# Kernel tuning notes

Hardware: AMD Instinct MI355X
Metric: run time of the kernel (lower is better)

Reference implementation:

```python
import jax, jax.numpy as jnp
import numpy as np
from jax import lax

B, N, NUM_Q, H = 16, 64, 256, 64


def setup_inputs() -> dict:
    key = jax.random.key(0)
    ks = jax.random.split(key, 12)
    s = 0.05
    return {
        "q": jax.random.randint(ks[0], (B, N), 0, NUM_Q),
        "r": jax.random.randint(ks[1], (B, N), 0, 2),
        "x_emb": jax.random.normal(ks[2], (2 * NUM_Q, H), jnp.float32) * s,
        "q_emb": jax.random.normal(ks[3], (NUM_Q, H), jnp.float32) * s,
        "init_h": jax.random.normal(ks[4], (NUM_Q, H), jnp.float32) * s,
        "w1": jax.random.normal(ks[5], (2 * H, H), jnp.float32) * s,
        "b1": jnp.zeros((H,), jnp.float32),
        "w2": jax.random.normal(ks[6], (H, H), jnp.float32) * s,
        "b2": jnp.zeros((H,), jnp.float32),
        "w_ih": jax.random.normal(ks[7], (3 * H, 2 * H), jnp.float32) * s,
        "w_hh": jax.random.normal(ks[8], (3 * H, H), jnp.float32) * s,
        "b_ih": jnp.zeros((3 * H,), jnp.float32),
        "b_hh": jnp.zeros((3 * H,), jnp.float32),
        "bias": jnp.zeros((1, NUM_Q, 1), jnp.float32),
        "out_w": jax.random.normal(ks[9], (H,), jnp.float32) * s,
        "theta": jnp.asarray(0.0, jnp.float32),
    }


def reference(q, r, x_emb, q_emb, init_h, w1, b1, w2, b2, w_ih, w_hh, b_ih, b_hh, bias, out_w, theta):
    xe = x_emb[q + NUM_Q * r]                          # [B,N,H]
    mask = jax.nn.one_hot(q, NUM_Q, dtype=xe.dtype)    # [B,N,Q] one-hot of answered KC
    ht0 = jnp.broadcast_to(init_h, (B, NUM_Q, H))

    def gru_seq(x):
        # torch nn.GRU(batch_first=True) scanned over the num_q axis, h0 = 0.
        # x: [B,Q,2H] -> [B,Q,H]; gate order (r, z, n).
        gi = jnp.einsum('bqi,gi->bqg', x, w_ih) + b_ih  # [B,Q,3H]

        def cell(h, gi_t):
            gh = h @ w_hh.T + b_hh
            i_r, i_z, i_n = jnp.split(gi_t, 3, axis=-1)
            h_r, h_z, h_n = jnp.split(gh, 3, axis=-1)
            rg = jax.nn.sigmoid(i_r + h_r)
            zg = jax.nn.sigmoid(i_z + h_z)
            ng = jnp.tanh(i_n + rg * h_n)
            hn = (1.0 - zg) * ng + zg * h
            return hn, hn

        _, hs = lax.scan(cell, jnp.zeros((B, H), x.dtype), jnp.swapaxes(gi, 0, 1))
        return jnp.swapaxes(hs, 0, 1)

    def step(ht, inp):
        xe_t, m_t = inp                                  # [B,H], [B,Q]
        m3 = m_t[..., None]
        # aggregate: answered KC gets [h, x_emb], others get [h, q_emb]
        tail = m3 * xe_t[:, None, :] + (1.0 - m3) * q_emb[None]
        ht_cat = jnp.concatenate([ht, tail], axis=-1)    # [B,Q,2H]
        # f_self MLP (dropout = identity in eval); f_neighbor undefined in
        # source (pass) -> shared MLP stand-in, so m = mlp(ht_cat) everywhere.
        m = jnp.maximum(ht_cat @ w1 + b1, 0.0) @ w2 + b2
        ht_new = gru_seq(jnp.concatenate([m, ht], axis=-1))
        return ht_new, ht_new

    _, hs = lax.scan(step, ht0, (jnp.swapaxes(xe, 0, 1), jnp.swapaxes(mask, 0, 1)))
    h_full = jnp.concatenate([ht0[None], hs], axis=0).transpose(1, 0, 2, 3)  # [B,N+1,Q,H]

    # decayed-softmax attention over the growing history, vectorized over t.
    rate = jnp.exp(theta)
    sim = jnp.einsum('btd,cd->btc', q_emb[q], q_emb)     # [B,tau,Q]
    idx = jnp.arange(N)
    dt = idx[:, None] - idx[None, :]                     # t - tau, [N,N]
    decay = jnp.exp(-rate * jnp.maximum(dt, 0).astype(sim.dtype))
    neg = jnp.finfo(sim.dtype).min
    scores = jnp.where((dt >= 0)[None, :, :, None],
                       decay[None, :, :, None] * sim[:, None, :, :], neg)  # [B,t,tau,Q]
    alpha = jax.nn.softmax(scores, axis=2)               # softmax over history tau
    hread = jnp.einsum('btuc,bucf->btcf', alpha, h_full[:, :N])
    h_cur = h_full[:, 1:]                                # state after step t
    logits = jnp.einsum('btcf,f->btc', h_cur + hread, out_w) + bias.reshape(1, 1, NUM_Q)
    y = jax.nn.sigmoid(logits)                           # [B,N,Q]
    return y, h_full
```

## Files before the change

### kernel.cpp

```cpp
#include <hip/hip_runtime.h>
#include <math.h>

#define WS_CB     0
#define WS_QE1    192
#define WS_XE1    16576
#define WS_G      82112
#define WS_HW     147648
#define WS_U16    413888
#define WS_WHH16  422080
#define WS_W2M16  428224
#define WS_GFLAG  442560

typedef _Float16 h2 __attribute__((ext_vector_type(2)));

#if defined(__has_builtin)
#if __has_builtin(__builtin_amdgcn_fdot2)
#define FDOT2(a,b,c) __builtin_amdgcn_fdot2((a),(b),(c),false)
#endif
#endif
#ifndef FDOT2
__device__ inline float fdot2_sw(h2 a, h2 b, float c){ return c + (float)a[0]*(float)b[0] + (float)a[1]*(float)b[1]; }
#define FDOT2(a,b,c) fdot2_sw((a),(b),(c))
#endif

__device__ inline h2 H2(unsigned u){ union{unsigned x; h2 h;} v; v.x=u; return v.h; }
__device__ inline unsigned short F2H(float f){ union{_Float16 h; unsigned short s;} v; v.h=(_Float16)f; return v.s; }
__device__ inline unsigned PACK2(float a, float b){ return (unsigned)F2H(a) | ((unsigned)F2H(b)<<16); }

#define F32(X,A) X(A,0)X(A,1)X(A,2)X(A,3)X(A,4)X(A,5)X(A,6)X(A,7)X(A,8)X(A,9)X(A,10)X(A,11)X(A,12)X(A,13)X(A,14)X(A,15)X(A,16)X(A,17)X(A,18)X(A,19)X(A,20)X(A,21)X(A,22)X(A,23)X(A,24)X(A,25)X(A,26)X(A,27)X(A,28)X(A,29)X(A,30)X(A,31)
#define DCL1(W,K) h2 W##_##K;
#define DECLW(W) F32(DCL1,W)
#define LD1(W,K) W##_##K = H2(_wb[K]);
#define LOADW(W,BASE) { const unsigned* _wb=(BASE); F32(LD1,W) }
#define DT1(W,K) _acc = FDOT2(W##_##K, H2(RC##K), _acc);
#define DOTW(ACC,W) { float _acc=(ACC); F32(DT1,W) (ACC)=_acc; }
#define RC0 qq0.x
#define RC1 qq0.y
#define RC2 qq0.z
#define RC3 qq0.w
#define RC4 qq1.x
#define RC5 qq1.y
#define RC6 qq1.z
#define RC7 qq1.w
#define RC8 qq2.x
#define RC9 qq2.y
#define RC10 qq2.z
#define RC11 qq2.w
#define RC12 qq3.x
#define RC13 qq3.y
#define RC14 qq3.z
#define RC15 qq3.w
#define RC16 qq4.x
#define RC17 qq4.y
#define RC18 qq4.z
#define RC19 qq4.w
#define RC20 qq5.x
#define RC21 qq5.y
#define RC22 qq5.z
#define RC23 qq5.w
#define RC24 qq6.x
#define RC25 qq6.y
#define RC26 qq6.z
#define RC27 qq6.w
#define RC28 qq7.x
#define RC29 qq7.y
#define RC30 qq7.z
#define RC31 qq7.w
#define LOADROW(P) { const uint4* _rp=(const uint4*)(P); qq0=_rp[0];qq1=_rp[1];qq2=_rp[2];qq3=_rp[3];qq4=_rp[4];qq5=_rp[5];qq6=_rp[6];qq7=_rp[7]; }

#define POLLGE(F,T) do{ while(*(volatile int*)&(F) < (T)) {} asm volatile("" ::: "memory"); }while(0)

__global__ __launch_bounds__(256) void kPrep(
    const int* __restrict__ q, const int* __restrict__ r,
    const float* __restrict__ x_emb, const float* __restrict__ q_emb,
    const float* __restrict__ init_h, const float* __restrict__ w1,
    const float* __restrict__ b1, const float* __restrict__ w2,
    const float* __restrict__ b2, const float* __restrict__ w_ih,
    const float* __restrict__ w_hh, const float* __restrict__ b_ih,
    float* __restrict__ ws, float* __restrict__ h_full)
{
  int idx = blockIdx.x*256 + threadIdx.x;
  unsigned* wsu = (unsigned*)ws;
  if (idx < 192) {
    int g = idx; float s = b_ih[g];
    for (int j=0;j<64;j++) s += b2[j]*w_ih[g*128+j];
    ws[WS_CB+g] = s;
  } else if (idx < 16576) {
    int e = idx-192; int c = e>>6, i = e&63;
    float s = b1[i];
    for (int k=0;k<64;k++) s += q_emb[c*64+k]*w1[(64+k)*64+i];
    ws[WS_QE1+e] = s;
  } else if (idx < 82112) {
    int e = idx-16576; int bt = e>>6, i = e&63;
    int row = q[bt] + 256*r[bt];
    float s = b1[i];
    for (int k=0;k<64;k++) s += x_emb[row*64+k]*w1[(64+k)*64+i];
    ws[WS_XE1+e] = s;
  } else if (idx < 147648) {
    int e = idx-82112; int a = e>>8, cc = e&255;
    float s = 0.f;
    for (int d=0;d<64;d++) s += q_emb[a*64+d]*q_emb[cc*64+d];
    ws[WS_G+e] = s;
  } else if (idx < 409792) {
    int e = idx-147648; int bb = e>>14, cf = e&16383;
    h_full[(size_t)bb*65*16384 + cf] = init_h[cf];
  } else if (idx < 417984) {
    int e = idx-409792; int rr = e>>5, d = e&31;
    float v0, v1;
    if (rr < 64) { v0 = w1[(2*d)*64+rr];   v1 = w1[(2*d+1)*64+rr]; }
    else { int g = rr-64; v0 = w_ih[g*128+64+2*d]; v1 = w_ih[g*128+64+2*d+1]; }
    wsu[WS_U16+e] = PACK2(v0,v1);
  } else if (idx < 424128) {
    int e = idx-417984; int g = e>>5, d = e&31;
    wsu[WS_WHH16+e] = PACK2(w_hh[g*64+2*d], w_hh[g*64+2*d+1]);
  } else if (idx < 430272) {
    int e = idx-424128; int g = e>>5, d = e&31;
    float s0=0.f, s1=0.f;
    for (int j=0;j<64;j++){ float wij = w_ih[g*128+j]; s0 += w2[(2*d)*64+j]*wij; s1 += w2[(2*d+1)*64+j]*wij; }
    wsu[WS_W2M16+e] = PACK2(s0,s1);
  }
}

__global__ __launch_bounds__(512,2) void kA(
    const int* __restrict__ q, const float* __restrict__ b_hh,
    float* __restrict__ ws, float* __restrict__ h_full)
{
  __shared__ __align__(16) unsigned short h16s[4][16][64];
  __shared__ __align__(16) unsigned short a16s[4][8][64];
  __shared__ __align__(16) unsigned short inbox[16][64];
  __shared__ __align__(16) float4 gi4s[4][8][64];
  __shared__ float h32s[4][8][64];
  __shared__ int flgH[4], p2s[4], ioPr[4];

  const int bid=blockIdx.x, b=bid&15, tg=bid>>4;
  const int tid=threadIdx.x, w=tid>>6, lane=tid&63;
  const bool isA = (w<4);
  const int i = isA? w : w-4;
  const int t = tg*4 + i;

  const unsigned* U16  = (const unsigned*)ws + WS_U16;
  const unsigned* WH16 = (const unsigned*)ws + WS_WHH16;
  const unsigned* WM16 = (const unsigned*)ws + WS_W2M16;
  const float* qe1 = ws + WS_QE1;
  const float* xe1 = ws + WS_XE1;
  const float* cb  = ws + WS_CB;
  unsigned* gflag = (unsigned*)ws + WS_GFLAG;

  if (tid<4){ flgH[tid]=0; p2s[tid]=0; ioPr[tid]=0; }
  if (isA) h16s[i][15][lane]=0;
  __syncthreads();

  uint4 qq0,qq1,qq2,qq3,qq4,qq5,qq6,qq7;

  if (isA) {
    DECLW(wrq) DECLW(wzq) DECLW(wnq) DECLW(mrq) DECLW(mzq)
    LOADW(wrq, WH16+lane*32)
    LOADW(wzq, WH16+(64+lane)*32)
    LOADW(wnq, WH16+(128+lane)*32)
    LOADW(mrq, WM16+lane*32)
    LOADW(mzq, WM16+(64+lane)*32)
    const float bhr=b_hh[lane], bhz=b_hh[64+lane], bhn=b_hh[128+lane];
    float hreg=0.f;
    for (int c=0;c<256;c++){
      if (((c&7)==0) && i<3) POLLGE(p2s[i+1], c-8);
      if ((c&3)==0) POLLGE(ioPr[i], c-4);
      LOADROW(h16s[i][(c+15)&15])
      float ghr=bhr, ghz=bhz, ghn=bhn;
      DOTW(ghr,wrq) DOTW(ghz,wzq) DOTW(ghn,wnq)
      POLLGE(p2s[i], c+1);
      float4 gv = gi4s[i][c&7][lane];
      LOADROW(a16s[i][c&7])
      float g2r=0.f, g2z=0.f;
      DOTW(g2r,mrq) DOTW(g2z,mzq)
      float rg = 1.f/(1.f+__expf(-(gv.x+g2r+ghr)));
      float zg = 1.f/(1.f+__expf(-(gv.y+g2z+ghz)));
      float xn = gv.z + rg*ghn;
      float e2 = __expf(2.f*xn);
      float ng = 1.f-2.f/(e2+1.f);
      hreg = zg*hreg + (1.f-zg)*ng;
      h16s[i][c&15][lane]=F2H(hreg);
      h32s[i][c&7][lane]=hreg;
      asm volatile("s_waitcnt lgkmcnt(0)" ::: "memory");
      if (lane==0) *(volatile int*)&flgH[i]=c+1;
    }
  } else {
    DECLW(u0q) DECLW(u1q) DECLW(u2q) DECLW(u3q) DECLW(w2q)
    LOADW(u0q, U16+lane*32)
    LOADW(u1q, U16+(64+lane)*32)
    LOADW(u2q, U16+(128+lane)*32)
    LOADW(u3q, U16+(192+lane)*32)
    LOADW(w2q, WM16+(128+lane)*32)
    const float cbr=cb[lane], cbz=cb[64+lane], cbn=cb[128+lane];
    const int qrow=q[b*64+t];
    const float xr=xe1[(b*64+t)*64+lane];
    const float* hfp = h_full + (size_t)(b*65+4*tg)*16384;
    float* hfoF = h_full + (size_t)(b*65+t+1)*16384;
    unsigned* hfoU = (unsigned*)hfoF;
    unsigned* gfp = gflag + (b*16+tg-1);
    unsigned* gfc = gflag + (b*16+tg);
    const bool pubG = (i==3) && (tg<15);
    unsigned gv=0; int pfrow=0, cp=0;
    float e1cur = (qrow==0)? xr : qe1[lane];
    float prP=0.f,pzP=0.f,pnP=0.f;

    for (int s=0;s<=256;s++){
      if ((s&3)==0) POLLGE(flgH[i], s-4);
      float e1n=0.f;
      if (s<255) e1n = ((s+1)==qrow)? xr : qe1[(s+1)*64+lane];
      float pr=0.f,pz=0.f,pn=0.f;
      if (s<=255){
        if (i==0){
          while (pfrow<=s){
            if (tg>0){
              while (gv < (unsigned)(pfrow+1)){
                gv = __hip_atomic_load(gfp,__ATOMIC_RELAXED,__HIP_MEMORY_SCOPE_AGENT);
                if (gv < (unsigned)(pfrow+1)) __builtin_amdgcn_s_sleep(1);
              }
              union{unsigned u; float f;} cv;
              cv.u = __hip_atomic_load((const unsigned*)&hfp[pfrow*64+lane],__ATOMIC_RELAXED,__HIP_MEMORY_SCOPE_AGENT);
              inbox[pfrow&15][lane]=F2H(cv.f);
            } else {
              inbox[pfrow&15][lane]=F2H(hfp[pfrow*64+lane]);
            }
            pfrow++;
          }
          if (pfrow<=s+8){
            bool can=(tg==0);
            if (tg>0){
              if (gv>=(unsigned)(pfrow+1)) can=true;
              else if ((s&1)==0){ gv=__hip_atomic_load(gfp,__ATOMIC_RELAXED,__HIP_MEMORY_SCOPE_AGENT); can = gv>=(unsigned)(pfrow+1); }
            }
            if (can){
              if (tg>0){
                union{unsigned u; float f;} cv;
                cv.u = __hip_atomic_load((const unsigned*)&hfp[pfrow*64+lane],__ATOMIC_RELAXED,__HIP_MEMORY_SCOPE_AGENT);
                inbox[pfrow&15][lane]=F2H(cv.f);
              } else {
                inbox[pfrow&15][lane]=F2H(hfp[pfrow*64+lane]);
              }
              pfrow++;
            }
          }
        } else {
          POLLGE(flgH[i-1], s+1);
        }
        LOADROW( (i==0)? inbox[s&15] : h16s[i-1][s&15] )
        float m1=e1cur; pr=cbr; pz=cbz; pn=cbn;
        DOTW(m1,u0q) DOTW(pr,u1q) DOTW(pz,u2q) DOTW(pn,u3q)
        a16s[i][s&7][lane]=F2H(fmaxf(m1,0.f));
      }
      if (s>=1){
        LOADROW(a16s[i][(s-1)&7])
        float g2n=0.f; DOTW(g2n,w2q)
        gi4s[i][(s-1)&7][lane]=make_float4(prP,pzP,pnP+g2n,0.f);
      }
      asm volatile("s_waitcnt lgkmcnt(0)" ::: "memory");
      if (lane==0) *(volatile int*)&p2s[i]=s;
      prP=pr; pzP=pz; pnP=pn; e1cur=e1n;
      int av=*(volatile int*)&flgH[i];
      asm volatile("" ::: "memory");
      int nc=0;
      while (cp<av && nc<2){
        float hv=h32s[i][cp&7][lane];
        if (i==3){ union{float f; unsigned u;} cu; cu.f=hv;
          __hip_atomic_store(&hfoU[cp*64+lane],cu.u,__ATOMIC_RELAXED,__HIP_MEMORY_SCOPE_AGENT);
        } else hfoF[cp*64+lane]=hv;
        cp++; nc++;
        if ((cp&3)==0){
          *(volatile int*)&ioPr[i]=cp;
          if (pubG){ asm volatile("s_waitcnt vmcnt(0)" ::: "memory");
            if (lane==0) __hip_atomic_store(gfc,(unsigned)cp,__ATOMIC_RELAXED,__HIP_MEMORY_SCOPE_AGENT); }
        }
      }
    }
    while (cp<256){
      POLLGE(flgH[i], cp+1);
      float hv=h32s[i][cp&7][lane];
      if (i==3){ union{float f; unsigned u;} cu; cu.f=hv;
        __hip_atomic_store(&hfoU[cp*64+lane],cu.u,__ATOMIC_RELAXED,__HIP_MEMORY_SCOPE_AGENT);
      } else hfoF[cp*64+lane]=hv;
      cp++;
      if ((cp&3)==0){
        *(volatile int*)&ioPr[i]=cp;
        if (pubG){ asm volatile("s_waitcnt vmcnt(0)" ::: "memory");
          if (lane==0) __hip_atomic_store(gfc,(unsigned)cp,__ATOMIC_RELAXED,__HIP_MEMORY_SCOPE_AGENT); }
      }
    }
  }
}

__global__ __launch_bounds__(256) void kHw(const float* __restrict__ h_full,
    const float* __restrict__ out_w, float* __restrict__ hw)
{
  __shared__ float ow[64];
  if (threadIdx.x < 64) ow[threadIdx.x] = out_w[threadIdx.x];
  __syncthreads();
  const int blk = blockIdx.x, c = threadIdx.x;
  const float* hp = h_full + ((size_t)blk*256 + c)*64;
  float s = 0.f;
  #pragma unroll
  for (int f=0; f<64; f++) s += hp[f]*ow[f];
  hw[blk*256+c] = s;
}

__global__ __launch_bounds__(256) void kY(const int* __restrict__ q,
    const float* __restrict__ ws, const float* __restrict__ bias,
    const float* __restrict__ theta, float* __restrict__ y)
{
  const float* G  = ws + WS_G;
  const float* hw = ws + WS_HW;
  const int b = blockIdx.x >> 2, tq = blockIdx.x & 3;
  const int c = threadIdx.x;
  __shared__ float siml[64][256];
  for (int u=0; u<64; u++) {
    int qq = q[b*64+u];
    siml[u][c] = G[qq*256+c];
  }
  __syncthreads();
  const float rate = __expf(theta[0]);
  const float bv = bias[c];
  const float* hwb = hw + b*65*256;
  for (int tt=0; tt<16; tt++) {
    const int t = tq*16+tt;
    float mx = -1e30f;
    for (int u=0; u<=t; u++) {
      float s = __expf(-rate*(float)(t-u))*siml[u][c];
      mx = fmaxf(mx, s);
    }
    float se = 0.f, sw = 0.f;
    for (int u=0; u<=t; u++) {
      float s = __expf(-rate*(float)(t-u))*siml[u][c];
      float e = __expf(s-mx);
      se += e; sw += e*hwb[u*256+c];
    }
    float lg = hwb[(t+1)*256+c] + sw/se + bv;
    y[(b*64+t)*256+c] = 1.f/(1.f+__expf(-lg));
  }
}

extern "C" void kernel_launch(void* const* d_in, const int* in_sizes, int n_in,
                              void* d_out, int out_size, void* d_ws, size_t ws_size,
                              hipStream_t stream)
{
  (void)in_sizes; (void)n_in; (void)out_size; (void)ws_size;
  const int*   q      = (const int*)  d_in[0];
  const int*   r      = (const int*)  d_in[1];
  const float* x_emb  = (const float*)d_in[2];
  const float* q_emb  = (const float*)d_in[3];
  const float* init_h = (const float*)d_in[4];
  const float* w1     = (const float*)d_in[5];
  const float* b1     = (const float*)d_in[6];
  const float* w2     = (const float*)d_in[7];
  const float* b2     = (const float*)d_in[8];
  const float* w_ih   = (const float*)d_in[9];
  const float* w_hh   = (const float*)d_in[10];
  const float* b_ih   = (const float*)d_in[11];
  const float* b_hh   = (const float*)d_in[12];
  const float* bias   = (const float*)d_in[13];
  const float* out_w  = (const float*)d_in[14];
  const float* theta  = (const float*)d_in[15];

  float* out    = (float*)d_out;
  float* y      = out;
  float* h_full = out + 262144;
  float* ws     = (float*)d_ws;

  hipMemsetAsync((unsigned*)ws + WS_GFLAG, 0, 256*sizeof(unsigned), stream);
  kPrep<<<1681,256,0,stream>>>(q,r,x_emb,q_emb,init_h,w1,b1,w2,b2,w_ih,w_hh,b_ih,ws,h_full);
  {
    void* ka[] = { (void*)&q, (void*)&b_hh, (void*)&ws, (void*)&h_full };
    hipError_t e = hipLaunchCooperativeKernel((const void*)kA, dim3(256), dim3(512), ka, 0, stream);
    if (e != hipSuccess) {
      kA<<<dim3(256),dim3(512),0,stream>>>(q,b_hh,ws,h_full);
    }
  }
  kHw<<<1040,256,0,stream>>>(h_full, out_w, ws + WS_HW);
  kY<<<64,256,0,stream>>>(q, ws, bias, theta, y);
}
```

Measured before the change: 795.8 us.

## Stage GRU weight matrices in LDS instead of register-resident fp16 weights

Moves the ten 64x64 fp16 weight blocks used by the recurrent kernel from per-thread registers (160 VGPRs of weights per wave) into a dynamically allocated LDS buffer laid out for uint4 reads, and replaces the unrolled register dot products with LDS-fed fdot2 loops. This frees registers and drops the two-blocks-per-CU launch bound. The recurrence wave now polls the producer flag every other step instead of every step. The cost is extra LDS bandwidth and latency on every dot product along the serial critical path, plus about 137 KB of LDS per block.

Result: slower. 1.148 ms (+44.3%).

```diff
diff --git a/kernel.cpp b/kernel.cpp
--- a/kernel.cpp
+++ b/kernel.cpp
@@ -27,48 +27,25 @@
 __device__ inline unsigned short F2H(float f){ union{_Float16 h; unsigned short s;} v; v.h=(_Float16)f; return v.s; }
 __device__ inline unsigned PACK2(float a, float b){ return (unsigned)F2H(a) | ((unsigned)F2H(b)<<16); }
 
-#define F32(X,A) X(A,0)X(A,1)X(A,2)X(A,3)X(A,4)X(A,5)X(A,6)X(A,7)X(A,8)X(A,9)X(A,10)X(A,11)X(A,12)X(A,13)X(A,14)X(A,15)X(A,16)X(A,17)X(A,18)X(A,19)X(A,20)X(A,21)X(A,22)X(A,23)X(A,24)X(A,25)X(A,26)X(A,27)X(A,28)X(A,29)X(A,30)X(A,31)
-#define DCL1(W,K) h2 W##_##K;
-#define DECLW(W) F32(DCL1,W)
-#define LD1(W,K) W##_##K = H2(_wb[K]);
-#define LOADW(W,BASE) { const unsigned* _wb=(BASE); F32(LD1,W) }
-#define DT1(W,K) _acc = FDOT2(W##_##K, H2(RC##K), _acc);
-#define DOTW(ACC,W) { float _acc=(ACC); F32(DT1,W) (ACC)=_acc; }
-#define RC0 qq0.x
-#define RC1 qq0.y
-#define RC2 qq0.z
-#define RC3 qq0.w
-#define RC4 qq1.x
-#define RC5 qq1.y
-#define RC6 qq1.z
-#define RC7 qq1.w
-#define RC8 qq2.x
-#define RC9 qq2.y
-#define RC10 qq2.z
-#define RC11 qq2.w
-#define RC12 qq3.x
-#define RC13 qq3.y
-#define RC14 qq3.z
-#define RC15 qq3.w
-#define RC16 qq4.x
-#define RC17 qq4.y
-#define RC18 qq4.z
-#define RC19 qq4.w
-#define RC20 qq5.x
-#define RC21 qq5.y
-#define RC22 qq5.z
-#define RC23 qq5.w
-#define RC24 qq6.x
-#define RC25 qq6.y
-#define RC26 qq6.z
-#define RC27 qq6.w
-#define RC28 qq7.x
-#define RC29 qq7.y
-#define RC30 qq7.z
-#define RC31 qq7.w
+#define POLLGE(F,T) do{ while(*(volatile int*)&(F) < (T)) {} asm volatile("" ::: "memory"); }while(0)
+
+#define LW_WT    0
+#define LW_H16   20480
+#define LW_A16   22528
+#define LW_INB   23552
+#define LW_GI4   24064
+#define LW_H32   32256
+#define LW_FLG   34304
+#define LDS_WORDS 34320
+#define LDS_BYTES (LDS_WORDS*4)
+
+#define DQB(Q,D4) { uint4 _w=_wp[(D4)*64+lane]; \
+  _a=FDOT2(H2(_w.x),H2(Q.x),_a); _a=FDOT2(H2(_w.y),H2(Q.y),_a); \
+  _a=FDOT2(H2(_w.z),H2(Q.z),_a); _a=FDOT2(H2(_w.w),H2(Q.w),_a); }
+#define DOTL(ACC,UIDX) { const uint4* _wp=(const uint4*)(ldsbuf+(UIDX)*2048); float _a=(ACC); \
+  DQB(qq0,0) DQB(qq1,1) DQB(qq2,2) DQB(qq3,3) DQB(qq4,4) DQB(qq5,5) DQB(qq6,6) DQB(qq7,7) (ACC)=_a; }
+
 #define LOADROW(P) { const uint4* _rp=(const uint4*)(P); qq0=_rp[0];qq1=_rp[1];qq2=_rp[2];qq3=_rp[3];qq4=_rp[4];qq5=_rp[5];qq6=_rp[6];qq7=_rp[7]; }
-
-#define POLLGE(F,T) do{ while(*(volatile int*)&(F) < (T)) {} asm volatile("" ::: "memory"); }while(0)
 
 __global__ __launch_bounds__(256) void kPrep(
     const int* __restrict__ q, const int* __restrict__ r,
@@ -121,16 +98,11 @@
   }
 }
 
-__global__ __launch_bounds__(512,2) void kA(
+__global__ __launch_bounds__(512) void kA(
     const int* __restrict__ q, const float* __restrict__ b_hh,
     float* __restrict__ ws, float* __restrict__ h_full)
 {
-  __shared__ __align__(16) unsigned short h16s[4][16][64];
-  __shared__ __align__(16) unsigned short a16s[4][8][64];
-  __shared__ __align__(16) unsigned short inbox[16][64];
-  __shared__ __align__(16) float4 gi4s[4][8][64];
-  __shared__ float h32s[4][8][64];
-  __shared__ int flgH[4], p2s[4], ioPr[4];
+  extern __shared__ unsigned ldsbuf[];
 
   const int bid=blockIdx.x, b=bid&15, tg=bid>>4;
   const int tid=threadIdx.x, w=tid>>6, lane=tid&63;
@@ -146,50 +118,60 @@
   const float* cb  = ws + WS_CB;
   unsigned* gflag = (unsigned*)ws + WS_GFLAG;
 
-  if (tid<4){ flgH[tid]=0; p2s[tid]=0; ioPr[tid]=0; }
-  if (isA) h16s[i][15][lane]=0;
+  unsigned short* h16s = (unsigned short*)(ldsbuf + LW_H16);
+  unsigned short* a16s = (unsigned short*)(ldsbuf + LW_A16);
+  unsigned short* inbox= (unsigned short*)(ldsbuf + LW_INB);
+  float4* gi4s = (float4*)(ldsbuf + LW_GI4);
+  float*  h32s = (float*)(ldsbuf + LW_H32);
+  int* FLG = (int*)(ldsbuf + LW_FLG);
+  int* flgH = FLG; int* p2s = FLG+4; int* ioPr = FLG+8;
+
+  for (int idx = tid; idx < 20480; idx += 512) {
+    int unit = idx>>11, ww = idx&2047;
+    int d4 = (ww>>8)&7, g = (ww>>2)&63, sub = ww&3;
+    int d = d4*4+sub;
+    unsigned v;
+    if (unit < 4)      v = U16 [(unit*64+g)*32 + d];
+    else if (unit==4)  v = WM16[(128+g)*32 + d];
+    else if (unit==5)  v = WM16[(g)*32 + d];
+    else if (unit==6)  v = WM16[(64+g)*32 + d];
+    else if (unit==7)  v = WH16[(g)*32 + d];
+    else if (unit==8)  v = WH16[(64+g)*32 + d];
+    else               v = WH16[(128+g)*32 + d];
+    ldsbuf[idx] = v;
+  }
+  if (tid<12) FLG[tid]=0;
+  if (isA) h16s[(i*16+15)*64 + lane] = 0;
   __syncthreads();
 
   uint4 qq0,qq1,qq2,qq3,qq4,qq5,qq6,qq7;
 
   if (isA) {
-    DECLW(wrq) DECLW(wzq) DECLW(wnq) DECLW(mrq) DECLW(mzq)
-    LOADW(wrq, WH16+lane*32)
-    LOADW(wzq, WH16+(64+lane)*32)
-    LOADW(wnq, WH16+(128+lane)*32)
-    LOADW(mrq, WM16+lane*32)
-    LOADW(mzq, WM16+(64+lane)*32)
     const float bhr=b_hh[lane], bhz=b_hh[64+lane], bhn=b_hh[128+lane];
     float hreg=0.f;
     for (int c=0;c<256;c++){
       if (((c&7)==0) && i<3) POLLGE(p2s[i+1], c-8);
       if ((c&3)==0) POLLGE(ioPr[i], c-4);
-      LOADROW(h16s[i][(c+15)&15])
+      LOADROW(&h16s[(i*16+((c+15)&15))*64])
       float ghr=bhr, ghz=bhz, ghn=bhn;
-      DOTW(ghr,wrq) DOTW(ghz,wzq) DOTW(ghn,wnq)
-      POLLGE(p2s[i], c+1);
-      float4 gv = gi4s[i][c&7][lane];
-      LOADROW(a16s[i][c&7])
+      DOTL(ghr,7) DOTL(ghz,8) DOTL(ghn,9)
+      if ((c&1)==0) { int tg2=c+2; if (tg2>256) tg2=256; POLLGE(p2s[i], tg2); }
+      float4 gv = gi4s[(i*8+(c&7))*64 + lane];
+      LOADROW(&a16s[(i*8+(c&7))*64])
       float g2r=0.f, g2z=0.f;
-      DOTW(g2r,mrq) DOTW(g2z,mzq)
+      DOTL(g2r,5) DOTL(g2z,6)
       float rg = 1.f/(1.f+__expf(-(gv.x+g2r+ghr)));
       float zg = 1.f/(1.f+__expf(-(gv.y+g2z+ghz)));
       float xn = gv.z + rg*ghn;
       float e2 = __expf(2.f*xn);
       float ng = 1.f-2.f/(e2+1.f);
       hreg = zg*hreg + (1.f-zg)*ng;
-      h16s[i][c&15][lane]=F2H(hreg);
-      h32s[i][c&7][lane]=hreg;
+      h16s[(i*16+(c&15))*64 + lane]=F2H(hreg);
+      h32s[(i*8+(c&7))*64 + lane]=hreg;
       asm volatile("s_waitcnt lgkmcnt(0)" ::: "memory");
       if (lane==0) *(volatile int*)&flgH[i]=c+1;
     }
   } else {
-    DECLW(u0q) DECLW(u1q) DECLW(u2q) DECLW(u3q) DECLW(w2q)
-    LOADW(u0q, U16+lane*32)
-    LOADW(u1q, U16+(64+lane)*32)
-    LOADW(u2q, U16+(128+lane)*32)
-    LOADW(u3q, U16+(192+lane)*32)
-    LOADW(w2q, WM16+(128+lane)*32)
     const float cbr=cb[lane], cbz=cb[64+lane], cbn=cb[128+lane];
     const int qrow=q[b*64+t];
     const float xr=xe1[(b*64+t)*64+lane];
@@ -218,9 +200,9 @@
               }
               union{unsigned u; float f;} cv;
               cv.u = __hip_atomic_load((const unsigned*)&hfp[pfrow*64+lane],__ATOMIC_RELAXED,__HIP_MEMORY_SCOPE_AGENT);
-              inbox[pfrow&15][lane]=F2H(cv.f);
+              inbox[(pfrow&15)*64+lane]=F2H(cv.f);
             } else {
-              inbox[pfrow&15][lane]=F2H(hfp[pfrow*64+lane]);
+              inbox[(pfrow&15)*64+lane]=F2H(hfp[pfrow*64+lane]);
             }
             pfrow++;
           }
@@ -234,9 +216,9 @@
               if (tg>0){
                 union{unsigned u; float f;} cv;
                 cv.u = __hip_atomic_load((const unsigned*)&hfp[pfrow*64+lane],__ATOMIC_RELAXED,__HIP_MEMORY_SCOPE_AGENT);
-                inbox[pfrow&15][lane]=F2H(cv.f);
+                inbox[(pfrow&15)*64+lane]=F2H(cv.f);
               } else {
-                inbox[pfrow&15][lane]=F2H(hfp[pfrow*64+lane]);
+                inbox[(pfrow&15)*64+lane]=F2H(hfp[pfrow*64+lane]);
               }
               pfrow++;
             }
@@ -244,15 +226,15 @@
         } else {
           POLLGE(flgH[i-1], s+1);
         }
-        LOADROW( (i==0)? inbox[s&15] : h16s[i-1][s&15] )
+        LOADROW( (i==0)? &inbox[(s&15)*64] : &h16s[((i-1)*16+(s&15))*64] )
         float m1=e1cur; pr=cbr; pz=cbz; pn=cbn;
-        DOTW(m1,u0q) DOTW(pr,u1q) DOTW(pz,u2q) DOTW(pn,u3q)
-        a16s[i][s&7][lane]=F2H(fmaxf(m1,0.f));
+        DOTL(m1,0) DOTL(pr,1) DOTL(pz,2) DOTL(pn,3)
+        a16s[(i*8+(s&7))*64+lane]=F2H(fmaxf(m1,0.f));
       }
       if (s>=1){
-        LOADROW(a16s[i][(s-1)&7])
-        float g2n=0.f; DOTW(g2n,w2q)
-        gi4s[i][(s-1)&7][lane]=make_float4(prP,pzP,pnP+g2n,0.f);
+        LOADROW(&a16s[(i*8+((s-1)&7))*64])
+        float g2n=0.f; DOTL(g2n,4)
+        gi4s[(i*8+((s-1)&7))*64+lane]=make_float4(prP,pzP,pnP+g2n,0.f);
       }
       asm volatile("s_waitcnt lgkmcnt(0)" ::: "memory");
       if (lane==0) *(volatile int*)&p2s[i]=s;
@@ -261,7 +243,7 @@
       asm volatile("" ::: "memory");
       int nc=0;
       while (cp<av && nc<2){
-        float hv=h32s[i][cp&7][lane];
+        float hv=h32s[(i*8+(cp&7))*64+lane];
         if (i==3){ union{float f; unsigned u;} cu; cu.f=hv;
           __hip_atomic_store(&hfoU[cp*64+lane],cu.u,__ATOMIC_RELAXED,__HIP_MEMORY_SCOPE_AGENT);
         } else hfoF[cp*64+lane]=hv;
@@ -275,7 +257,7 @@
     }
     while (cp<256){
       POLLGE(flgH[i], cp+1);
-      float hv=h32s[i][cp&7][lane];
+      float hv=h32s[(i*8+(cp&7))*64+lane];
       if (i==3){ union{float f; unsigned u;} cu; cu.f=hv;
         __hip_atomic_store(&hfoU[cp*64+lane],cu.u,__ATOMIC_RELAXED,__HIP_MEMORY_SCOPE_AGENT);
       } else hfoF[cp*64+lane]=hv;
@@ -368,10 +350,13 @@
   hipMemsetAsync((unsigned*)ws + WS_GFLAG, 0, 256*sizeof(unsigned), stream);
   kPrep<<<1681,256,0,stream>>>(q,r,x_emb,q_emb,init_h,w1,b1,w2,b2,w_ih,w_hh,b_ih,ws,h_full);
   {
+    static int attr_done = 0;
+    (void)attr_done;
+    hipFuncSetAttribute((const void*)kA, hipFuncAttributeMaxDynamicSharedMemorySize, LDS_BYTES);
     void* ka[] = { (void*)&q, (void*)&b_hh, (void*)&ws, (void*)&h_full };
-    hipError_t e = hipLaunchCooperativeKernel((const void*)kA, dim3(256), dim3(512), ka, 0, stream);
+    hipError_t e = hipLaunchCooperativeKernel((const void*)kA, dim3(256), dim3(512), ka, LDS_BYTES, stream);
     if (e != hipSuccess) {
-      kA<<<dim3(256),dim3(512),0,stream>>>(q,b_hh,ws,h_full);
+      kA<<<dim3(256),dim3(512),LDS_BYTES,stream>>>(q,b_hh,ws,h_full);
     }
   }
   kHw<<<1040,256,0,stream>>>(h_full, out_w, ws + WS_HW);
```
